# Kernel tuning notes

Hardware: AMD Instinct MI355X
Metric: run time of the kernel (lower is better)

## Reference

```python
import jax, jax.numpy as jnp
import numpy as np

NF = 64   # num_feat
DG = 8    # deformable_groups (also conv groups)
B, H, W = 4, 96, 96
K = 9     # 3x3 kernel positions


def _conv(x, w, b, padding=1, dilation=1, groups=1):
    out = jax.lax.conv_general_dilated(
        x, w, (1, 1), [(padding, padding), (padding, padding)],
        rhs_dilation=(dilation, dilation),
        dimension_numbers=('NCHW', 'OIHW', 'NCHW'),
        feature_group_count=groups)
    return out + b[None, :, None, None]


def _lrelu(t):
    return jnp.where(t >= 0, t, 0.1 * t)


def _cat_align(a, b):
    # channel-interleaved concat: [a0,b0,a1,b1,...]
    Bn, k, h, w = a.shape
    return jnp.stack([a, b], axis=2).reshape(Bn, 2 * k, h, w)


def _deform_conv(x, offset, mask, weight, bias, dilation, padding):
    # DCNv2 modulated deformable conv, stride 1.
    Bn, C, h, w = x.shape
    Cpg = C // DG
    off = offset.reshape(Bn, DG, K, 2, h, w)          # (dy, dx) per group/kernel pos
    m = mask.reshape(Bn, DG, K, h, w)
    ky = (jnp.repeat(jnp.arange(3), 3) * dilation - padding).astype(x.dtype)  # (K,)
    kx = (jnp.tile(jnp.arange(3), 3) * dilation - padding).astype(x.dtype)
    hs = jnp.arange(h, dtype=x.dtype)
    ws = jnp.arange(w, dtype=x.dtype)
    py = off[:, :, :, 0] + ky[None, None, :, None, None] + hs[None, None, None, :, None]
    px = off[:, :, :, 1] + kx[None, None, :, None, None] + ws[None, None, None, None, :]
    y0f = jnp.floor(py); x0f = jnp.floor(px)
    ly = (py - y0f)[:, :, None]  # broadcast over Cpg
    lx = (px - x0f)[:, :, None]
    y0 = y0f.astype(jnp.int32); x0 = x0f.astype(jnp.int32)
    xg = x.reshape(Bn, DG, Cpg, h * w)

    def gather(yi, xi):
        inb = ((yi >= 0) & (yi < h) & (xi >= 0) & (xi < w))
        idx = (jnp.clip(yi, 0, h - 1) * w + jnp.clip(xi, 0, w - 1)).reshape(Bn, DG, 1, K * h * w)
        v = jnp.take_along_axis(xg, jnp.broadcast_to(idx, (Bn, DG, Cpg, K * h * w)), axis=3)
        return v.reshape(Bn, DG, Cpg, K, h, w) * inb[:, :, None].astype(x.dtype)

    v00 = gather(y0, x0); v01 = gather(y0, x0 + 1)
    v10 = gather(y0 + 1, x0); v11 = gather(y0 + 1, x0 + 1)
    val = (v00 * (1 - ly) * (1 - lx) + v01 * (1 - ly) * lx
           + v10 * ly * (1 - lx) + v11 * ly * lx) * m[:, :, None]
    sampled = val.reshape(Bn, C, K, h, w)
    out = jnp.einsum('bckhw,ock->bohw', sampled, weight.reshape(weight.shape[0], C, K))
    return out + bias[None, :, None, None]


def _dcn(x, off_feat, om_w, om_b, w, b, dilation):
    pad = dilation  # int(3/2)*dilation
    out = _conv(off_feat, om_w, om_b, padding=pad, dilation=dilation)
    o1, o2, msk = jnp.split(out, 3, axis=1)
    offset = jnp.concatenate([o1, o2], axis=1)
    mask = jax.nn.sigmoid(msk)
    return _deform_conv(x, offset, mask, w, b, dilation, pad)


def setup_inputs() -> dict:
    key = jax.random.key(0)
    ks = iter(jax.random.split(key, 64))
    def rn(shape, s=0.05):
        return jax.random.normal(next(ks), shape, jnp.float32) * s
    d = {}
    d['nbr_feat'] = jax.random.normal(next(ks), (B, NF, H, W), jnp.float32)
    d['ref_feat'] = jax.random.normal(next(ks), (B, NF, H, W), jnp.float32)
    for lv, has3 in [('l3', False), ('l2', True), ('l1', True)]:
        d[f'oc1_w_{lv}'] = rn((NF, 2 * NF // DG, 3, 3)); d[f'oc1_b_{lv}'] = rn((NF,))
        oc2_in = 2 * NF if has3 else NF
        d[f'oc2_w_{lv}'] = rn((NF, oc2_in // DG, 3, 3)); d[f'oc2_b_{lv}'] = rn((NF,))
        if has3:
            d[f'oc3_w_{lv}'] = rn((NF, NF // DG, 3, 3)); d[f'oc3_b_{lv}'] = rn((NF,))
            d[f'fc_w_{lv}'] = rn((NF, 2 * NF // DG, 3, 3)); d[f'fc_b_{lv}'] = rn((NF,))
        d[f'om_w_{lv}'] = rn((DG * 3 * K, NF, 3, 3), 0.01); d[f'om_b_{lv}'] = rn((DG * 3 * K,), 0.01)
        d[f'dcn_w_{lv}'] = rn((NF, NF, 3, 3)); d[f'dcn_b_{lv}'] = rn((NF,))
    d['cas_oc1_w'] = rn((NF, 2 * NF // DG, 3, 3)); d['cas_oc1_b'] = rn((NF,))
    d['cas_oc2_w'] = rn((NF, NF // DG, 3, 3)); d['cas_oc2_b'] = rn((NF,))
    d['cas_om_w'] = rn((DG * 3 * K, NF, 3, 3), 0.01); d['cas_om_b'] = rn((DG * 3 * K,), 0.01)
    d['cas_w'] = rn((NF, NF, 3, 3)); d['cas_b'] = rn((NF,))
    return d


def reference(nbr_feat, ref_feat,
              oc1_w_l3, oc1_b_l3, oc2_w_l3, oc2_b_l3, om_w_l3, om_b_l3, dcn_w_l3, dcn_b_l3,
              oc1_w_l2, oc1_b_l2, oc2_w_l2, oc2_b_l2, oc3_w_l2, oc3_b_l2, fc_w_l2, fc_b_l2,
              om_w_l2, om_b_l2, dcn_w_l2, dcn_b_l2,
              oc1_w_l1, oc1_b_l1, oc2_w_l1, oc2_b_l1, oc3_w_l1, oc3_b_l1, fc_w_l1, fc_b_l1,
              om_w_l1, om_b_l1, dcn_w_l1, dcn_b_l1,
              cas_oc1_w, cas_oc1_b, cas_oc2_w, cas_oc2_b, cas_om_w, cas_om_b, cas_w, cas_b):
    # level 3 (dilation 5)
    off = _lrelu(_conv(_cat_align(nbr_feat, ref_feat), oc1_w_l3, oc1_b_l3, groups=DG))
    off = _lrelu(_conv(off, oc2_w_l3, oc2_b_l3, groups=DG))
    feat = _lrelu(_dcn(nbr_feat, off, om_w_l3, om_b_l3, dcn_w_l3, dcn_b_l3, 5))
    to, tf = off, feat
    # level 2 (dilation 3)
    off = _lrelu(_conv(_cat_align(nbr_feat, ref_feat), oc1_w_l2, oc1_b_l2, groups=DG))
    off = _lrelu(_conv(_cat_align(off, to), oc2_w_l2, oc2_b_l2, groups=DG))
    off = _lrelu(_conv(off, oc3_w_l2, oc3_b_l2, groups=DG))
    feat = _dcn(nbr_feat, off, om_w_l2, om_b_l2, dcn_w_l2, dcn_b_l2, 3)
    feat = _lrelu(_conv(_cat_align(feat, tf), fc_w_l2, fc_b_l2, groups=DG))
    to, tf = off, feat
    # level 1 (dilation 1), no lrelu on feat
    off = _lrelu(_conv(_cat_align(nbr_feat, ref_feat), oc1_w_l1, oc1_b_l1, groups=DG))
    off = _lrelu(_conv(_cat_align(off, to), oc2_w_l1, oc2_b_l1, groups=DG))
    off = _lrelu(_conv(off, oc3_w_l1, oc3_b_l1, groups=DG))
    feat = _dcn(nbr_feat, off, om_w_l1, om_b_l1, dcn_w_l1, dcn_b_l1, 1)
    feat = _conv(_cat_align(feat, tf), fc_w_l1, fc_b_l1, groups=DG)
    # cascade
    off = _cat_align(feat, ref_feat)
    off = _lrelu(_conv(_lrelu(_conv(off, cas_oc1_w, cas_oc1_b, groups=DG)), cas_oc2_w, cas_oc2_b, groups=DG))
    feat = _lrelu(_dcn(feat, off, cas_om_w, cas_om_b, cas_w, cas_b, 1))
    return feat
```

## Files before the change

kernel.cpp:

```cpp
#include <hip/hip_runtime.h>

#define BATCH 4
#define NFEAT 64
#define DGRP 8
#define HH 96
#define WW 96
#define HWP (HH*WW)

typedef short short4a __attribute__((ext_vector_type(4)));
typedef short short8 __attribute__((ext_vector_type(8)));
typedef float f32x4 __attribute__((ext_vector_type(4)));
typedef float f32x16 __attribute__((ext_vector_type(16)));

__device__ inline short f2bf(float f) {
  union { float f; unsigned u; } v; v.f = f;
  unsigned r = v.u + 0x7fff + ((v.u >> 16) & 1);
  return (short)(r >> 16);
}
__device__ inline float bf2f(short s) {
  return __uint_as_float(((unsigned)(unsigned short)s) << 16);
}

__global__ __launch_bounds__(256) void prep_om(
    const float* __restrict__ s0, const float* __restrict__ s1,
    const float* __restrict__ s2, const float* __restrict__ s3,
    short* __restrict__ dst) {
  int gid = blockIdx.x * 256 + threadIdx.x;
  if (gid >= 4 * 147456) return;
  int t = gid / 147456, r = gid % 147456;
  int tile = r / 18432, r2 = r % 18432;
  int kk = r2 / 512, r3 = r2 % 512;
  int lane = r3 / 8, j = r3 % 8;
  int col = lane & 31, half = lane >> 5;
  int oc = tile * 32 + col;
  int k = kk * 16 + half * 8 + j;
  int p = k >> 6, c = k & 63;
  const float* s = (t == 0) ? s0 : (t == 1) ? s1 : (t == 2) ? s2 : s3;
  float v = (oc < 216) ? s[(size_t)oc * 576 + c * 9 + p] : 0.f;
  dst[gid] = f2bf(v);
}

__global__ __launch_bounds__(256) void prep_dcnw(
    const float* __restrict__ s0, const float* __restrict__ s1,
    const float* __restrict__ s2, const float* __restrict__ s3,
    short* __restrict__ dst) {
  int gid = blockIdx.x * 256 + threadIdx.x;
  if (gid >= 4 * 36864) return;
  int t = gid / 36864, r = gid % 36864;
  int tile = r / 18432, r2 = r % 18432;
  int kk = r2 / 512, r3 = r2 % 512;
  int lane = r3 / 8, j = r3 % 8;
  int col = lane & 31, half = lane >> 5;
  int oc = tile * 32 + col;
  int k = kk * 16 + half * 8 + j;
  int p = k >> 6, c = k & 63;
  const float* s = (t == 0) ? s0 : (t == 1) ? s1 : (t == 2) ? s2 : s3;
  dst[gid] = f2bf(s[(size_t)oc * 576 + c * 9 + p]);
}

struct GwArgs {
  const float* src[12];
  int cat[12];
  int base[13];
};

__global__ __launch_bounds__(256) void prep_gw(GwArgs a, short* __restrict__ dst) {
  int gid = blockIdx.x * 256 + threadIdx.x;
  if (gid >= a.base[12]) return;
  int t = 0;
  while (gid >= a.base[t + 1]) ++t;
  int r = gid - a.base[t];
  const float* s = a.src[t];
  const int tsz = a.cat[t] ? 4608 : 2560;
  int tile = r / tsz, r2 = r % tsz;
  int kk = r2 / 512, r3 = r2 % 512;
  int lane = r3 >> 3, j = r3 & 7;
  int m = lane & 15, quad = lane >> 4;
  int oc = tile * 16 + m;
  int j32 = quad * 8 + j;
  float val = 0.f;
  if (a.cat[t]) {
    int gsel = j32 >> 4, ssel = (j32 >> 3) & 1, ch8 = j32 & 7;
    if (gsel == (m >> 3)) val = s[oc * 144 + (2 * ch8 + ssel) * 9 + kk];
  } else {
    int tapsel = j32 >> 4, gsel = (j32 >> 3) & 1, ch8 = j32 & 7;
    int p = 2 * kk + tapsel;
    if (p < 9 && gsel == (m >> 3)) val = s[oc * 72 + ch8 * 9 + p];
  }
  dst[gid] = f2bf(val);
}

__global__ __launch_bounds__(256) void transpose_bf16(
    const float* __restrict__ in0, short* __restrict__ out0,
    const float* __restrict__ in1, short* __restrict__ out1) {
  const float* in = blockIdx.z ? in1 : in0;
  short* out = blockIdx.z ? out1 : out0;
  __shared__ float s[64][65];
  const int p0 = blockIdx.x * 64;
  const int b = blockIdx.y;
  const int tx = threadIdx.x, ty = threadIdx.y;
  for (int c = ty; c < 64; c += 4)
    s[c][tx] = in[((size_t)b * NFEAT + c) * HWP + p0 + tx];
  __syncthreads();
  for (int p = ty; p < 64; p += 4)
    out[((size_t)b * HWP + p0 + p) * NFEAT + tx] = f2bf(s[tx][p]);
}

template <bool CAT, bool LRELU>
__device__ __forceinline__ void gconv_body(
    const short* __restrict__ in0, const short* __restrict__ in1,
    const short* __restrict__ Wsh, const float* __restrict__ bias,
    short* __restrict__ out, int pixbase, int b) {
  const int lane = threadIdx.x, t = threadIdx.y;
  const int n = lane & 15, quad = lane >> 4;
  constexpr int NKK = CAT ? 9 : 5;

  short8 A[NKK];
#pragma unroll
  for (int kk = 0; kk < NKK; ++kk)
    A[kk] = *(const short8*)(Wsh + ((size_t)(t * NKK + kk) * 64 + lane) * 8);

  const short* sb;
  if (CAT) {
    sb = ((quad & 1) ? in1 : in0) + (size_t)b * HWP * 64 + (2 * t + (quad >> 1)) * 8;
  } else {
    sb = in0 + (size_t)b * HWP * 64 + (2 * t + (quad & 1)) * 8;
  }

  f32x4 acc[2] = {};
#pragma unroll
  for (int nt = 0; nt < 2; ++nt) {
    const int pix = pixbase + nt * 16 + n;
    const int yp = pix / WW, xp = pix % WW;
#pragma unroll
    for (int kk = 0; kk < NKK; ++kk) {
      const int p = CAT ? kk : (2 * kk + (quad >> 1));
      short8 B = {0, 0, 0, 0, 0, 0, 0, 0};
      if (p < 9) {
        const int sy = yp + p / 3 - 1, sx = xp + p % 3 - 1;
        if (((unsigned)sy < (unsigned)HH) && ((unsigned)sx < (unsigned)WW))
          B = *(const short8*)(sb + (size_t)(sy * WW + sx) * 64);
      }
      acc[nt] = __builtin_amdgcn_mfma_f32_16x16x32_bf16(A[kk], B, acc[nt], 0, 0, 0);
    }
  }

  const int ocb = t * 16 + quad * 4;
  const float b0 = bias[ocb], b1 = bias[ocb + 1], b2 = bias[ocb + 2], b3 = bias[ocb + 3];
#pragma unroll
  for (int nt = 0; nt < 2; ++nt) {
    float v0 = acc[nt][0] + b0, v1 = acc[nt][1] + b1;
    float v2 = acc[nt][2] + b2, v3 = acc[nt][3] + b3;
    if (LRELU) {
      v0 = (v0 >= 0.f) ? v0 : 0.1f * v0;
      v1 = (v1 >= 0.f) ? v1 : 0.1f * v1;
      v2 = (v2 >= 0.f) ? v2 : 0.1f * v2;
      v3 = (v3 >= 0.f) ? v3 : 0.1f * v3;
    }
    short4a pk = {f2bf(v0), f2bf(v1), f2bf(v2), f2bf(v3)};
    *(short4a*)(out + ((size_t)b * HWP + pixbase + nt * 16 + n) * 64 + ocb) = pk;
  }
}

template <bool CAT, bool LRELU>
__global__ __launch_bounds__(256) void gconv_mfma(
    const short* __restrict__ in0, const short* __restrict__ in1,
    const short* __restrict__ Wsh, const float* __restrict__ bias,
    short* __restrict__ out) {
  gconv_body<CAT, LRELU>(in0, in1, Wsh, bias, out, blockIdx.x * 32, blockIdx.y);
}

struct Oc1Args {
  const short* W[3];
  const float* bias[3];
  short* out[3];
};

__global__ __launch_bounds__(256) void gconv_oc1x3(
    const short* __restrict__ in0, const short* __restrict__ in1, Oc1Args a) {
  const int job = blockIdx.z;
  gconv_body<true, true>(in0, in1, a.W[job], a.bias[job], a.out[job],
                         blockIdx.x * 32, blockIdx.y);
}

#define BPITCH 324
template <int D>
__global__ __launch_bounds__(256) void omconv_mfma(
    const short* __restrict__ pixT,
    const short* __restrict__ Wsh,
    const float* __restrict__ bias,
    short* __restrict__ out) {
  const int lane = threadIdx.x;
  const int w = threadIdx.y;
  const int lid = w * 64 + lane;
  const int col = lane & 31, half = lane >> 5;
  const int pixbase = blockIdx.x * 64;
  const int b = blockIdx.y;

  __shared__ short Bs[64 * BPITCH];

  const short* aP0 = Wsh + ((size_t)(w * 36) * 64) * 8 + (size_t)lane * 8;
  const short* aP1 = Wsh + ((size_t)((w + 4) * 36) * 64) * 8 + (size_t)lane * 8;
  const short* pixb = pixT + (size_t)b * HWP * 64;

  f32x16 acc00 = {}, acc01 = {}, acc10 = {}, acc11 = {};

  for (int ph = 0; ph < 2; ++ph) {
    const int ntap = ph ? 4 : 5, pbase = ph ? 5 : 0, kbase = ph ? 20 : 0;
    if (ph) __syncthreads();
    const int nchunk = 64 * ntap * 8;
    for (int i = lid; i < nchunk; i += 256) {
      int row = i / (ntap * 8), q = i % (ntap * 8);
      int p = pbase + (q >> 3), c8 = q & 7;
      int pix = pixbase + row;
      int yp = pix / WW, xp = pix % WW;
      int sy = yp + (p / 3 - 1) * D, sx = xp + (p % 3 - 1) * D;
      short4a lo = {0, 0, 0, 0}, hi = {0, 0, 0, 0};
      if (((unsigned)sy < (unsigned)HH) && ((unsigned)sx < (unsigned)WW)) {
        const short* src = pixb + (size_t)(sy * WW + sx) * 64 + c8 * 8;
        lo = *(const short4a*)src;
        hi = *(const short4a*)(src + 4);
      }
      short* dst = Bs + row * BPITCH + q * 8;
      *(short4a*)dst = lo;
      *(short4a*)(dst + 4) = hi;
    }
    __syncthreads();

    const int nkk = ntap * 4;
#pragma unroll 4
    for (int kk = 0; kk < nkk; ++kk) {
      const int kkg = kbase + kk;
      short8 A0 = *(const short8*)(aP0 + (size_t)kkg * 512);
      short8 A1 = *(const short8*)(aP1 + (size_t)kkg * 512);
      const short* b0 = Bs + col * BPITCH + kk * 16 + half * 8;
      const short* b1 = Bs + (32 + col) * BPITCH + kk * 16 + half * 8;
      short4a l0 = *(const short4a*)b0, h0 = *(const short4a*)(b0 + 4);
      short4a l1 = *(const short4a*)b1, h1 = *(const short4a*)(b1 + 4);
      short8 B0 = {l0[0], l0[1], l0[2], l0[3], h0[0], h0[1], h0[2], h0[3]};
      short8 B1 = {l1[0], l1[1], l1[2], l1[3], h1[0], h1[1], h1[2], h1[3]};
      acc00 = __builtin_amdgcn_mfma_f32_32x32x16_bf16(A0, B0, acc00, 0, 0, 0);
      acc01 = __builtin_amdgcn_mfma_f32_32x32x16_bf16(A0, B1, acc01, 0, 0, 0);
      acc10 = __builtin_amdgcn_mfma_f32_32x32x16_bf16(A1, B0, acc10, 0, 0, 0);
      acc11 = __builtin_amdgcn_mfma_f32_32x32x16_bf16(A1, B1, acc11, 0, 0, 0);
    }
  }

  const int pix0 = pixbase + col, pix1 = pixbase + 32 + col;
#pragma unroll
  for (int r = 0; r < 16; ++r) {
    const int rrow = (r & 3) + 8 * (r >> 2) + 4 * half;
    const int oc0 = w * 32 + rrow;
    const int oc1 = (w + 4) * 32 + rrow;
    const float bs0 = bias[oc0];
    out[((size_t)b * 216 + oc0) * HWP + pix0] = f2bf(acc00[r] + bs0);
    out[((size_t)b * 216 + oc0) * HWP + pix1] = f2bf(acc01[r] + bs0);
    if (oc1 < 216) {
      const float bs1 = bias[oc1];
      out[((size_t)b * 216 + oc1) * HWP + pix0] = f2bf(acc10[r] + bs1);
      out[((size_t)b * 216 + oc1) * HWP + pix1] = f2bf(acc11[r] + bs1);
    }
  }
}

template <int D, bool LRELU, bool PMOUT>
__global__ __launch_bounds__(256) void dcn_fused(
    const short* __restrict__ xT,
    const short* __restrict__ om,
    const short* __restrict__ Wd,
    const float* __restrict__ bias,
    void* __restrict__ outv) {
  __shared__ short Ls[36 * 512];
  __shared__ float red[2][64][17];
  const int tx = threadIdx.x, ty = threadIdx.y;
  const int pb = blockIdx.x, b = blockIdx.y;

  {
    const int px = tx, dg = ty;
    const int pix = pb * 32 + px;
    const int yp = pix / WW, xp = pix % WW;
    const size_t bOM = (size_t)b * 216 * HWP;
    const short* xb = xT + (size_t)b * HWP * 64 + dg * 8;
    short* Sp = Ls + (size_t)((dg & 1) * 32 + px) * 8;

#pragma unroll
    for (int k = 0; k < 9; ++k) {
      float dy = bf2f(om[bOM + (size_t)(dg * 18 + 2 * k) * HWP + pix]);
      float dxv = bf2f(om[bOM + (size_t)(dg * 18 + 2 * k + 1) * HWP + pix]);
      float mr = bf2f(om[bOM + (size_t)(144 + dg * 9 + k) * HWP + pix]);
      float m = 1.f / (1.f + __expf(-mr));
      float py = (float)(yp + (k / 3 - 1) * D) + dy;
      float px_ = (float)(xp + (k % 3 - 1) * D) + dxv;
      float y0f = floorf(py), x0f = floorf(px_);
      float ly = py - y0f, lx = px_ - x0f;
      int y0 = (int)y0f, x0 = (int)x0f;
      int y1 = y0 + 1, x1 = x0 + 1;
      bool vy0 = (unsigned)y0 < (unsigned)HH, vy1 = (unsigned)y1 < (unsigned)HH;
      bool vx0 = (unsigned)x0 < (unsigned)WW, vx1 = (unsigned)x1 < (unsigned)WW;
      int cy0 = min(max(y0, 0), HH - 1), cy1 = min(max(y1, 0), HH - 1);
      int cx0 = min(max(x0, 0), WW - 1), cx1 = min(max(x1, 0), WW - 1);
      float w00 = (vy0 && vx0) ? (1.f - ly) * (1.f - lx) * m : 0.f;
      float w01 = (vy0 && vx1) ? (1.f - ly) * lx * m : 0.f;
      float w10 = (vy1 && vx0) ? ly * (1.f - lx) * m : 0.f;
      float w11 = (vy1 && vx1) ? ly * lx * m : 0.f;
      short8 s00 = *(const short8*)(xb + (size_t)(cy0 * WW + cx0) * 64);
      short8 s01 = *(const short8*)(xb + (size_t)(cy0 * WW + cx1) * 64);
      short8 s10 = *(const short8*)(xb + (size_t)(cy1 * WW + cx0) * 64);
      short8 s11 = *(const short8*)(xb + (size_t)(cy1 * WW + cx1) * 64);
      short8 pk;
#pragma unroll
      for (int cl = 0; cl < 8; ++cl) {
        float v = w00 * bf2f(s00[cl]) + w01 * bf2f(s01[cl]) +
                  w10 * bf2f(s10[cl]) + w11 * bf2f(s11[cl]);
        pk[cl] = f2bf(v);
      }
      const int kk = k * 4 + (dg >> 1);
      *(short8*)(Sp + (size_t)kk * 512) = pk;
    }
  }
  __syncthreads();

  const int lid = ty * 32 + tx;
  const int lane = lid & 63, w = lid >> 6;
  const int col = lane & 31, half = lane >> 5;
  const int octile = w & 1, kh = w >> 1;
  const int pix = pb * 32 + col;

  const short* aP = Wd + ((size_t)(octile * 36) * 64 + lane) * 8;
  const short* bP = Ls + (size_t)lane * 8;

  f32x16 acc = {};
#pragma unroll 6
  for (int kk = 0; kk < 18; ++kk) {
    const int kkg = kh * 18 + kk;
    short8 A = *(const short8*)(aP + (size_t)kkg * 512);
    short8 B = *(const short8*)(bP + (size_t)kkg * 512);
    acc = __builtin_amdgcn_mfma_f32_32x32x16_bf16(A, B, acc, 0, 0, 0);
  }

  if (kh == 1) {
#pragma unroll
    for (int r = 0; r < 16; ++r) red[octile][lane][r] = acc[r];
  }
  __syncthreads();
  if (kh == 0) {
    if (PMOUT) {
      short* out = (short*)outv;
#pragma unroll
      for (int rg = 0; rg < 4; ++rg) {
        short4a pk;
#pragma unroll
        for (int i = 0; i < 4; ++i) {
          const int r = rg * 4 + i;
          const int oc = octile * 32 + i + 8 * rg + 4 * half;
          float v = acc[r] + red[octile][lane][r] + bias[oc];
          if (LRELU) v = (v >= 0.f) ? v : 0.1f * v;
          pk[i] = f2bf(v);
        }
        *(short4a*)(out + ((size_t)b * HWP + pix) * 64 + octile * 32 + 8 * rg + 4 * half) = pk;
      }
    } else {
      float* out = (float*)outv;
#pragma unroll
      for (int r = 0; r < 16; ++r) {
        const int oc = octile * 32 + (r & 3) + 8 * (r >> 2) + 4 * half;
        float v = acc[r] + red[octile][lane][r] + bias[oc];
        if (LRELU) v = (v >= 0.f) ? v : 0.1f * v;
        out[((size_t)b * NFEAT + oc) * HWP + pix] = v;
      }
    }
  }
}

extern "C" void kernel_launch(void* const* d_in, const int* in_sizes, int n_in,
                              void* d_out, int out_size, void* d_ws, size_t ws_size,
                              hipStream_t stream) {
  const float* nbr = (const float*)d_in[0];
  const float* ref = (const float*)d_in[1];
  auto f = [&](int i) { return (const float*)d_in[i]; };

  short* s0 = (short*)d_ws;
  const size_t PM = (size_t)BATCH * HWP * 64;
  short* omB = s0;
  short* refT = omB + 7962624;
  short* pmA = refT + PM;
  short* pmB = pmA + PM;
  short* pmC = pmB + PM;
  short* pmD = pmC + PM;
  short* pmE = pmD + PM;
  short* pmF = pmE + PM;
  short* pmG = pmF + PM;
  short* wbf = pmG + PM;
  short* wdcn = wbf + 589824;
  short* wgc = wdcn + 147456;
  short* nbrT = (short*)d_out;

  prep_om<<<(4 * 147456 + 255) / 256, 256, 0, stream>>>(f(6), f(18), f(30), f(38), wbf);
  prep_dcnw<<<(4 * 36864 + 255) / 256, 256, 0, stream>>>(f(8), f(20), f(32), f(40), wdcn);

  static const int gSrc[12] = {2, 4, 10, 12, 14, 16, 22, 24, 26, 28, 34, 36};
  static const int gCat[12] = {1, 0, 1, 1, 0, 1, 1, 1, 0, 1, 1, 0};
  GwArgs ga;
  int gb = 0;
  const short* wg[12];
  for (int t = 0; t < 12; ++t) {
    ga.src[t] = f(gSrc[t]);
    ga.cat[t] = gCat[t];
    ga.base[t] = gb;
    wg[t] = wgc + gb;
    gb += gCat[t] ? 18432 : 10240;
  }
  ga.base[12] = gb;
  prep_gw<<<(gb + 255) / 256, 256, 0, stream>>>(ga, wgc);

  short* wbf_l3 = wbf;
  short* wbf_l2 = wbf + 147456;
  short* wbf_l1 = wbf + 2 * 147456;
  short* wbf_cas = wbf + 3 * 147456;
  short* wd_l3 = wdcn;
  short* wd_l2 = wdcn + 36864;
  short* wd_l1 = wdcn + 2 * 36864;
  short* wd_cas = wdcn + 3 * 36864;

  dim3 gcGrid(288, BATCH), gcBlk(64, 4);
  dim3 oc1Grid(288, BATCH, 3);
  dim3 omGrid(144, BATCH), omBlk(64, 4);
  dim3 dfGrid(288, BATCH), dfBlk(32, 8);
  dim3 trGrid(HWP / 64, BATCH, 2), trBlk(64, 4);

  transpose_bf16<<<trGrid, trBlk, 0, stream>>>(nbr, nbrT, ref, refT);

  Oc1Args oa;
  oa.W[0] = wg[0]; oa.bias[0] = f(3);  oa.out[0] = pmA;
  oa.W[1] = wg[2]; oa.bias[1] = f(11); oa.out[1] = pmF;
  oa.W[2] = wg[6]; oa.bias[2] = f(23); oa.out[2] = pmG;
  gconv_oc1x3<<<oc1Grid, gcBlk, 0, stream>>>(nbrT, refT, oa);

  gconv_mfma<false, true><<<gcGrid, gcBlk, 0, stream>>>(pmA, nullptr, wg[1], f(5), pmB);
  omconv_mfma<5><<<omGrid, omBlk, 0, stream>>>(pmB, wbf_l3, f(7), omB);
  dcn_fused<5, true, true><<<dfGrid, dfBlk, 0, stream>>>(nbrT, omB, wd_l3, f(9), pmC);

  gconv_mfma<true, true><<<gcGrid, gcBlk, 0, stream>>>(pmF, pmB, wg[3], f(13), pmD);
  gconv_mfma<false, true><<<gcGrid, gcBlk, 0, stream>>>(pmD, nullptr, wg[4], f(15), pmE);
  omconv_mfma<3><<<omGrid, omBlk, 0, stream>>>(pmE, wbf_l2, f(19), omB);
  dcn_fused<3, false, true><<<dfGrid, dfBlk, 0, stream>>>(nbrT, omB, wd_l2, f(21), pmD);
  gconv_mfma<true, true><<<gcGrid, gcBlk, 0, stream>>>(pmD, pmC, wg[5], f(17), pmA);

  gconv_mfma<true, true><<<gcGrid, gcBlk, 0, stream>>>(pmG, pmE, wg[7], f(25), pmB);
  gconv_mfma<false, true><<<gcGrid, gcBlk, 0, stream>>>(pmB, nullptr, wg[8], f(27), pmC);
  omconv_mfma<1><<<omGrid, omBlk, 0, stream>>>(pmC, wbf_l1, f(31), omB);
  dcn_fused<1, false, true><<<dfGrid, dfBlk, 0, stream>>>(nbrT, omB, wd_l1, f(33), pmD);
  gconv_mfma<true, false><<<gcGrid, gcBlk, 0, stream>>>(pmD, pmA, wg[9], f(29), pmB);

  gconv_mfma<true, true><<<gcGrid, gcBlk, 0, stream>>>(pmB, refT, wg[10], f(35), pmC);
  gconv_mfma<false, true><<<gcGrid, gcBlk, 0, stream>>>(pmC, nullptr, wg[11], f(37), pmD);
  omconv_mfma<1><<<omGrid, omBlk, 0, stream>>>(pmD, wbf_cas, f(39), omB);
  dcn_fused<1, true, false><<<dfGrid, dfBlk, 0, stream>>>(pmB, omB, wd_cas, f(41), (float*)d_out);
}
```

Before: 526.7 us.

## Fuse offset/mask conv into deformable conv kernel via LDS handoff

Merges the separate offset/mask MFMA convolution kernel into the deformable conv kernel. Each 32-pixel block now computes its 216 offset/mask channels into shared memory and consumes them directly, instead of writing them to a global buffer and reading them back. This removes the global round trip of the 216-channel om tensor and one launch per level. In exchange, pixel tiles shrink from 64 to 32 per block for the om conv, so weight loads are reused less, and the larger shared footprint (about 51KB) may lower occupancy.

```diff
diff --git a/kernel.cpp b/kernel.cpp
--- a/kernel.cpp
+++ b/kernel.cpp
@@ -183,111 +183,93 @@
                          blockIdx.x * 32, blockIdx.y);
 }
 
-#define BPITCH 324
-template <int D>
-__global__ __launch_bounds__(256) void omconv_mfma(
-    const short* __restrict__ pixT,
-    const short* __restrict__ Wsh,
+#define OMPITCH 580
+#define OMLP 33
+
+template <int D, bool LRELU, bool PMOUT>
+__global__ __launch_bounds__(256) void omdcn_fused(
+    const short* __restrict__ omIn,
+    const short* __restrict__ xT,
+    const short* __restrict__ Wom,
+    const float* __restrict__ obias,
+    const short* __restrict__ Wd,
     const float* __restrict__ bias,
-    short* __restrict__ out) {
-  const int lane = threadIdx.x;
-  const int w = threadIdx.y;
-  const int lid = w * 64 + lane;
+    void* __restrict__ outv) {
+  __shared__ __align__(16) char smem[37120 + 14256];
+  short* Bs = (short*)smem;
+  short* Ls = (short*)smem;
+  short* om_lds = (short*)(smem + 37120);
+  float* red = (float*)(smem + 37120);
+
+  const int tx = threadIdx.x, ty = threadIdx.y;
+  const int lid = ty * 32 + tx;
+  const int lane = lid & 63, w = lid >> 6;
   const int col = lane & 31, half = lane >> 5;
-  const int pixbase = blockIdx.x * 64;
-  const int b = blockIdx.y;
-
-  __shared__ short Bs[64 * BPITCH];
-
-  const short* aP0 = Wsh + ((size_t)(w * 36) * 64) * 8 + (size_t)lane * 8;
-  const short* aP1 = Wsh + ((size_t)((w + 4) * 36) * 64) * 8 + (size_t)lane * 8;
-  const short* pixb = pixT + (size_t)b * HWP * 64;
-
-  f32x16 acc00 = {}, acc01 = {}, acc10 = {}, acc11 = {};
-
-  for (int ph = 0; ph < 2; ++ph) {
-    const int ntap = ph ? 4 : 5, pbase = ph ? 5 : 0, kbase = ph ? 20 : 0;
-    if (ph) __syncthreads();
-    const int nchunk = 64 * ntap * 8;
-    for (int i = lid; i < nchunk; i += 256) {
-      int row = i / (ntap * 8), q = i % (ntap * 8);
-      int p = pbase + (q >> 3), c8 = q & 7;
-      int pix = pixbase + row;
-      int yp = pix / WW, xp = pix % WW;
-      int sy = yp + (p / 3 - 1) * D, sx = xp + (p % 3 - 1) * D;
+  const int pb = blockIdx.x, b = blockIdx.y;
+  const int pixbase = pb * 32;
+
+  {
+    const short* pixb = omIn + (size_t)b * HWP * 64;
+#pragma unroll
+    for (int t = 0; t < 9; ++t) {
+      const int i = lid + t * 256;
+      const int row = i / 72, q = i % 72;
+      const int p = q >> 3, c8 = q & 7;
+      const int pix = pixbase + row;
+      const int yp = pix / WW, xp = pix % WW;
+      const int sy = yp + (p / 3 - 1) * D, sx = xp + (p % 3 - 1) * D;
       short4a lo = {0, 0, 0, 0}, hi = {0, 0, 0, 0};
       if (((unsigned)sy < (unsigned)HH) && ((unsigned)sx < (unsigned)WW)) {
         const short* src = pixb + (size_t)(sy * WW + sx) * 64 + c8 * 8;
         lo = *(const short4a*)src;
         hi = *(const short4a*)(src + 4);
       }
-      short* dst = Bs + row * BPITCH + q * 8;
+      short* dst = Bs + row * OMPITCH + q * 8;
       *(short4a*)dst = lo;
       *(short4a*)(dst + 4) = hi;
     }
-    __syncthreads();
-
-    const int nkk = ntap * 4;
+  }
+  __syncthreads();
+
+  {
+    const short* aP0 = Wom + ((size_t)(w * 36) * 64 + lane) * 8;
+    const short* aP1 = Wom + ((size_t)((w + 4) * 36) * 64 + lane) * 8;
+    const short* bbase = Bs + col * OMPITCH + half * 8;
+    f32x16 acc0 = {}, acc1 = {};
 #pragma unroll 4
-    for (int kk = 0; kk < nkk; ++kk) {
-      const int kkg = kbase + kk;
-      short8 A0 = *(const short8*)(aP0 + (size_t)kkg * 512);
-      short8 A1 = *(const short8*)(aP1 + (size_t)kkg * 512);
-      const short* b0 = Bs + col * BPITCH + kk * 16 + half * 8;
-      const short* b1 = Bs + (32 + col) * BPITCH + kk * 16 + half * 8;
-      short4a l0 = *(const short4a*)b0, h0 = *(const short4a*)(b0 + 4);
-      short4a l1 = *(const short4a*)b1, h1 = *(const short4a*)(b1 + 4);
-      short8 B0 = {l0[0], l0[1], l0[2], l0[3], h0[0], h0[1], h0[2], h0[3]};
-      short8 B1 = {l1[0], l1[1], l1[2], l1[3], h1[0], h1[1], h1[2], h1[3]};
-      acc00 = __builtin_amdgcn_mfma_f32_32x32x16_bf16(A0, B0, acc00, 0, 0, 0);
-      acc01 = __builtin_amdgcn_mfma_f32_32x32x16_bf16(A0, B1, acc01, 0, 0, 0);
-      acc10 = __builtin_amdgcn_mfma_f32_32x32x16_bf16(A1, B0, acc10, 0, 0, 0);
-      acc11 = __builtin_amdgcn_mfma_f32_32x32x16_bf16(A1, B1, acc11, 0, 0, 0);
-    }
-  }
-
-  const int pix0 = pixbase + col, pix1 = pixbase + 32 + col;
-#pragma unroll
-  for (int r = 0; r < 16; ++r) {
-    const int rrow = (r & 3) + 8 * (r >> 2) + 4 * half;
-    const int oc0 = w * 32 + rrow;
-    const int oc1 = (w + 4) * 32 + rrow;
-    const float bs0 = bias[oc0];
-    out[((size_t)b * 216 + oc0) * HWP + pix0] = f2bf(acc00[r] + bs0);
-    out[((size_t)b * 216 + oc0) * HWP + pix1] = f2bf(acc01[r] + bs0);
-    if (oc1 < 216) {
-      const float bs1 = bias[oc1];
-      out[((size_t)b * 216 + oc1) * HWP + pix0] = f2bf(acc10[r] + bs1);
-      out[((size_t)b * 216 + oc1) * HWP + pix1] = f2bf(acc11[r] + bs1);
-    }
-  }
-}
-
-template <int D, bool LRELU, bool PMOUT>
-__global__ __launch_bounds__(256) void dcn_fused(
-    const short* __restrict__ xT,
-    const short* __restrict__ om,
-    const short* __restrict__ Wd,
-    const float* __restrict__ bias,
-    void* __restrict__ outv) {
-  __shared__ short Ls[36 * 512];
-  __shared__ float red[2][64][17];
-  const int tx = threadIdx.x, ty = threadIdx.y;
-  const int pb = blockIdx.x, b = blockIdx.y;
+    for (int kk = 0; kk < 36; ++kk) {
+      const short* bp = bbase + kk * 16;
+      short4a l = *(const short4a*)bp, h = *(const short4a*)(bp + 4);
+      short8 B = {l[0], l[1], l[2], l[3], h[0], h[1], h[2], h[3]};
+      short8 A0 = *(const short8*)(aP0 + (size_t)kk * 512);
+      short8 A1 = *(const short8*)(aP1 + (size_t)kk * 512);
+      acc0 = __builtin_amdgcn_mfma_f32_32x32x16_bf16(A0, B, acc0, 0, 0, 0);
+      acc1 = __builtin_amdgcn_mfma_f32_32x32x16_bf16(A1, B, acc1, 0, 0, 0);
+    }
+#pragma unroll
+    for (int r = 0; r < 16; ++r) {
+      const int rrow = (r & 3) + 8 * (r >> 2) + 4 * half;
+      const int oc0 = w * 32 + rrow;
+      om_lds[oc0 * OMLP + col] = f2bf(acc0[r] + obias[oc0]);
+      const int oc1 = (w + 4) * 32 + rrow;
+      if (oc1 < 216)
+        om_lds[oc1 * OMLP + col] = f2bf(acc1[r] + obias[oc1]);
+    }
+  }
+  __syncthreads();
 
   {
     const int px = tx, dg = ty;
-    const int pix = pb * 32 + px;
+    const int pix = pixbase + px;
     const int yp = pix / WW, xp = pix % WW;
-    const size_t bOM = (size_t)b * 216 * HWP;
     const short* xb = xT + (size_t)b * HWP * 64 + dg * 8;
     short* Sp = Ls + (size_t)((dg & 1) * 32 + px) * 8;
 
 #pragma unroll
     for (int k = 0; k < 9; ++k) {
-      float dy = bf2f(om[bOM + (size_t)(dg * 18 + 2 * k) * HWP + pix]);
-      float dxv = bf2f(om[bOM + (size_t)(dg * 18 + 2 * k + 1) * HWP + pix]);
-      float mr = bf2f(om[bOM + (size_t)(144 + dg * 9 + k) * HWP + pix]);
+      float dy = bf2f(om_lds[(dg * 18 + 2 * k) * OMLP + px]);
+      float dxv = bf2f(om_lds[(dg * 18 + 2 * k + 1) * OMLP + px]);
+      float mr = bf2f(om_lds[(144 + dg * 9 + k) * OMLP + px]);
       float m = 1.f / (1.f + __expf(-mr));
       float py = (float)(yp + (k / 3 - 1) * D) + dy;
       float px_ = (float)(xp + (k % 3 - 1) * D) + dxv;
@@ -320,11 +302,8 @@
   }
   __syncthreads();
 
-  const int lid = ty * 32 + tx;
-  const int lane = lid & 63, w = lid >> 6;
-  const int col = lane & 31, half = lane >> 5;
   const int octile = w & 1, kh = w >> 1;
-  const int pix = pb * 32 + col;
+  const int pix = pixbase + col;
 
   const short* aP = Wd + ((size_t)(octile * 36) * 64 + lane) * 8;
   const short* bP = Ls + (size_t)lane * 8;
@@ -340,7 +319,7 @@
 
   if (kh == 1) {
 #pragma unroll
-    for (int r = 0; r < 16; ++r) red[octile][lane][r] = acc[r];
+    for (int r = 0; r < 16; ++r) red[(octile * 64 + lane) * 17 + r] = acc[r];
   }
   __syncthreads();
   if (kh == 0) {
@@ -353,7 +332,7 @@
         for (int i = 0; i < 4; ++i) {
           const int r = rg * 4 + i;
           const int oc = octile * 32 + i + 8 * rg + 4 * half;
-          float v = acc[r] + red[octile][lane][r] + bias[oc];
+          float v = acc[r] + red[(octile * 64 + lane) * 17 + r] + bias[oc];
           if (LRELU) v = (v >= 0.f) ? v : 0.1f * v;
           pk[i] = f2bf(v);
         }
@@ -364,7 +343,7 @@
 #pragma unroll
       for (int r = 0; r < 16; ++r) {
         const int oc = octile * 32 + (r & 3) + 8 * (r >> 2) + 4 * half;
-        float v = acc[r] + red[octile][lane][r] + bias[oc];
+        float v = acc[r] + red[(octile * 64 + lane) * 17 + r] + bias[oc];
         if (LRELU) v = (v >= 0.f) ? v : 0.1f * v;
         out[((size_t)b * NFEAT + oc) * HWP + pix] = v;
       }
@@ -424,8 +403,7 @@
 
   dim3 gcGrid(288, BATCH), gcBlk(64, 4);
   dim3 oc1Grid(288, BATCH, 3);
-  dim3 omGrid(144, BATCH), omBlk(64, 4);
-  dim3 dfGrid(288, BATCH), dfBlk(32, 8);
+  dim3 fGrid(288, BATCH), fBlk(32, 8);
   dim3 trGrid(HWP / 64, BATCH, 2), trBlk(64, 4);
 
   transpose_bf16<<<trGrid, trBlk, 0, stream>>>(nbr, nbrT, ref, refT);
@@ -437,23 +415,23 @@
   gconv_oc1x3<<<oc1Grid, gcBlk, 0, stream>>>(nbrT, refT, oa);
 
   gconv_mfma<false, true><<<gcGrid, gcBlk, 0, stream>>>(pmA, nullptr, wg[1], f(5), pmB);
-  omconv_mfma<5><<<omGrid, omBlk, 0, stream>>>(pmB, wbf_l3, f(7), omB);
-  dcn_fused<5, true, true><<<dfGrid, dfBlk, 0, stream>>>(nbrT, omB, wd_l3, f(9), pmC);
+  omdcn_fused<5, true, true><<<fGrid, fBlk, 0, stream>>>(
+      pmB, nbrT, wbf_l3, f(7), wd_l3, f(9), pmC);
 
   gconv_mfma<true, true><<<gcGrid, gcBlk, 0, stream>>>(pmF, pmB, wg[3], f(13), pmD);
   gconv_mfma<false, true><<<gcGrid, gcBlk, 0, stream>>>(pmD, nullptr, wg[4], f(15), pmE);
-  omconv_mfma<3><<<omGrid, omBlk, 0, stream>>>(pmE, wbf_l2, f(19), omB);
-  dcn_fused<3, false, true><<<dfGrid, dfBlk, 0, stream>>>(nbrT, omB, wd_l2, f(21), pmD);
+  omdcn_fused<3, false, true><<<fGrid, fBlk, 0, stream>>>(
+      pmE, nbrT, wbf_l2, f(19), wd_l2, f(21), pmD);
   gconv_mfma<true, true><<<gcGrid, gcBlk, 0, stream>>>(pmD, pmC, wg[5], f(17), pmA);
 
   gconv_mfma<true, true><<<gcGrid, gcBlk, 0, stream>>>(pmG, pmE, wg[7], f(25), pmB);
   gconv_mfma<false, true><<<gcGrid, gcBlk, 0, stream>>>(pmB, nullptr, wg[8], f(27), pmC);
-  omconv_mfma<1><<<omGrid, omBlk, 0, stream>>>(pmC, wbf_l1, f(31), omB);
-  dcn_fused<1, false, true><<<dfGrid, dfBlk, 0, stream>>>(nbrT, omB, wd_l1, f(33), pmD);
+  omdcn_fused<1, false, true><<<fGrid, fBlk, 0, stream>>>(
+      pmC, nbrT, wbf_l1, f(31), wd_l1, f(33), pmD);
   gconv_mfma<true, false><<<gcGrid, gcBlk, 0, stream>>>(pmD, pmA, wg[9], f(29), pmB);
 
   gconv_mfma<true, true><<<gcGrid, gcBlk, 0, stream>>>(pmB, refT, wg[10], f(35), pmC);
   gconv_mfma<false, true><<<gcGrid, gcBlk, 0, stream>>>(pmC, nullptr, wg[11], f(37), pmD);
-  omconv_mfma<1><<<omGrid, omBlk, 0, stream>>>(pmD, wbf_cas, f(39), omB);
-  dcn_fused<1, true, false><<<dfGrid, dfBlk, 0, stream>>>(pmB, omB, wd_cas, f(41), (float*)d_out);
-}
+  omdcn_fused<1, true, false><<<fGrid, fBlk, 0, stream>>>(
+      pmD, pmB, wbf_cas, f(39), wd_cas, f(41), (float*)d_out);
+}
```

New measurement: 546.1 us. 3.7% more time.

## Prefetch second omconv tap phase into registers; merge two independent gconvs into one launch

Applied to the files above, without the earlier changes.

The offset/mask conv kernel now issues the global loads for the second group of taps into registers before computing on the first group. Those values are written to shared memory only after the first MFMA phase, so load latency overlaps with compute. A custom barrier waits only on LDS counters and leaves global loads in flight. Separately, the level-2 feature conv and the level-1 offset conv are independent, so they now run as one launch split by blockIdx.z, removing a launch and letting their blocks share the GPU. The register prefetch adds VGPR pressure that could lower occupancy.

```diff
diff --git a/kernel.cpp b/kernel.cpp
--- a/kernel.cpp
+++ b/kernel.cpp
@@ -19,6 +19,12 @@
 }
 __device__ inline float bf2f(short s) {
   return __uint_as_float(((unsigned)(unsigned short)s) << 16);
+}
+
+__device__ __forceinline__ void barrier_keep_vmcnt() {
+  asm volatile("s_waitcnt lgkmcnt(0)" ::: "memory");
+  __builtin_amdgcn_s_barrier();
+  asm volatile("" ::: "memory");
 }
 
 __global__ __launch_bounds__(256) void prep_om(
@@ -183,6 +189,20 @@
                          blockIdx.x * 32, blockIdx.y);
 }
 
+struct Pair2Args {
+  const short* in0[2];
+  const short* in1[2];
+  const short* W[2];
+  const float* bias[2];
+  short* out[2];
+};
+
+__global__ __launch_bounds__(256) void gconv_pair(Pair2Args a) {
+  const int j = blockIdx.z;
+  gconv_body<true, true>(a.in0[j], a.in1[j], a.W[j], a.bias[j], a.out[j],
+                         blockIdx.x * 32, blockIdx.y);
+}
+
 #define BPITCH 324
 template <int D>
 __global__ __launch_bounds__(256) void omconv_mfma(
@@ -205,45 +225,85 @@
 
   f32x16 acc00 = {}, acc01 = {}, acc10 = {}, acc11 = {};
 
-  for (int ph = 0; ph < 2; ++ph) {
-    const int ntap = ph ? 4 : 5, pbase = ph ? 5 : 0, kbase = ph ? 20 : 0;
-    if (ph) __syncthreads();
-    const int nchunk = 64 * ntap * 8;
-    for (int i = lid; i < nchunk; i += 256) {
-      int row = i / (ntap * 8), q = i % (ntap * 8);
-      int p = pbase + (q >> 3), c8 = q & 7;
-      int pix = pixbase + row;
-      int yp = pix / WW, xp = pix % WW;
-      int sy = yp + (p / 3 - 1) * D, sx = xp + (p % 3 - 1) * D;
-      short4a lo = {0, 0, 0, 0}, hi = {0, 0, 0, 0};
-      if (((unsigned)sy < (unsigned)HH) && ((unsigned)sx < (unsigned)WW)) {
-        const short* src = pixb + (size_t)(sy * WW + sx) * 64 + c8 * 8;
-        lo = *(const short4a*)src;
-        hi = *(const short4a*)(src + 4);
-      }
-      short* dst = Bs + row * BPITCH + q * 8;
-      *(short4a*)dst = lo;
-      *(short4a*)(dst + 4) = hi;
-    }
-    __syncthreads();
-
-    const int nkk = ntap * 4;
+  for (int i = lid; i < 64 * 5 * 8; i += 256) {
+    int row = i / 40, q = i % 40;
+    int p = q >> 3, c8 = q & 7;
+    int pix = pixbase + row;
+    int yp = pix / WW, xp = pix % WW;
+    int sy = yp + (p / 3 - 1) * D, sx = xp + (p % 3 - 1) * D;
+    short4a lo = {0, 0, 0, 0}, hi = {0, 0, 0, 0};
+    if (((unsigned)sy < (unsigned)HH) && ((unsigned)sx < (unsigned)WW)) {
+      const short* src = pixb + (size_t)(sy * WW + sx) * 64 + c8 * 8;
+      lo = *(const short4a*)src;
+      hi = *(const short4a*)(src + 4);
+    }
+    short* dst = Bs + row * BPITCH + q * 8;
+    *(short4a*)dst = lo;
+    *(short4a*)(dst + 4) = hi;
+  }
+
+  short4a p1lo[8], p1hi[8];
+  int p1dst[8];
+#pragma unroll
+  for (int idx = 0; idx < 8; ++idx) {
+    int i = lid + idx * 256;
+    int row = i / 32, q = i % 32;
+    int p = 5 + (q >> 3), c8 = q & 7;
+    int pix = pixbase + row;
+    int yp = pix / WW, xp = pix % WW;
+    int sy = yp + (p / 3 - 1) * D, sx = xp + (p % 3 - 1) * D;
+    short4a lo = {0, 0, 0, 0}, hi = {0, 0, 0, 0};
+    if (((unsigned)sy < (unsigned)HH) && ((unsigned)sx < (unsigned)WW)) {
+      const short* src = pixb + (size_t)(sy * WW + sx) * 64 + c8 * 8;
+      lo = *(const short4a*)src;
+      hi = *(const short4a*)(src + 4);
+    }
+    p1lo[idx] = lo;
+    p1hi[idx] = hi;
+    p1dst[idx] = row * BPITCH + q * 8;
+  }
+  barrier_keep_vmcnt();
+
 #pragma unroll 4
-    for (int kk = 0; kk < nkk; ++kk) {
-      const int kkg = kbase + kk;
-      short8 A0 = *(const short8*)(aP0 + (size_t)kkg * 512);
-      short8 A1 = *(const short8*)(aP1 + (size_t)kkg * 512);
-      const short* b0 = Bs + col * BPITCH + kk * 16 + half * 8;
-      const short* b1 = Bs + (32 + col) * BPITCH + kk * 16 + half * 8;
-      short4a l0 = *(const short4a*)b0, h0 = *(const short4a*)(b0 + 4);
-      short4a l1 = *(const short4a*)b1, h1 = *(const short4a*)(b1 + 4);
-      short8 B0 = {l0[0], l0[1], l0[2], l0[3], h0[0], h0[1], h0[2], h0[3]};
-      short8 B1 = {l1[0], l1[1], l1[2], l1[3], h1[0], h1[1], h1[2], h1[3]};
-      acc00 = __builtin_amdgcn_mfma_f32_32x32x16_bf16(A0, B0, acc00, 0, 0, 0);
-      acc01 = __builtin_amdgcn_mfma_f32_32x32x16_bf16(A0, B1, acc01, 0, 0, 0);
-      acc10 = __builtin_amdgcn_mfma_f32_32x32x16_bf16(A1, B0, acc10, 0, 0, 0);
-      acc11 = __builtin_amdgcn_mfma_f32_32x32x16_bf16(A1, B1, acc11, 0, 0, 0);
-    }
+  for (int kk = 0; kk < 20; ++kk) {
+    short8 A0 = *(const short8*)(aP0 + (size_t)kk * 512);
+    short8 A1 = *(const short8*)(aP1 + (size_t)kk * 512);
+    const short* b0 = Bs + col * BPITCH + kk * 16 + half * 8;
+    const short* b1 = Bs + (32 + col) * BPITCH + kk * 16 + half * 8;
+    short4a l0 = *(const short4a*)b0, h0 = *(const short4a*)(b0 + 4);
+    short4a l1 = *(const short4a*)b1, h1 = *(const short4a*)(b1 + 4);
+    short8 B0 = {l0[0], l0[1], l0[2], l0[3], h0[0], h0[1], h0[2], h0[3]};
+    short8 B1 = {l1[0], l1[1], l1[2], l1[3], h1[0], h1[1], h1[2], h1[3]};
+    acc00 = __builtin_amdgcn_mfma_f32_32x32x16_bf16(A0, B0, acc00, 0, 0, 0);
+    acc01 = __builtin_amdgcn_mfma_f32_32x32x16_bf16(A0, B1, acc01, 0, 0, 0);
+    acc10 = __builtin_amdgcn_mfma_f32_32x32x16_bf16(A1, B0, acc10, 0, 0, 0);
+    acc11 = __builtin_amdgcn_mfma_f32_32x32x16_bf16(A1, B1, acc11, 0, 0, 0);
+  }
+  barrier_keep_vmcnt();
+
+#pragma unroll
+  for (int idx = 0; idx < 8; ++idx) {
+    short* dst = Bs + p1dst[idx];
+    *(short4a*)dst = p1lo[idx];
+    *(short4a*)(dst + 4) = p1hi[idx];
+  }
+  barrier_keep_vmcnt();
+
+#pragma unroll 4
+  for (int kk = 0; kk < 16; ++kk) {
+    const int kkg = 20 + kk;
+    short8 A0 = *(const short8*)(aP0 + (size_t)kkg * 512);
+    short8 A1 = *(const short8*)(aP1 + (size_t)kkg * 512);
+    const short* b0 = Bs + col * BPITCH + kk * 16 + half * 8;
+    const short* b1 = Bs + (32 + col) * BPITCH + kk * 16 + half * 8;
+    short4a l0 = *(const short4a*)b0, h0 = *(const short4a*)(b0 + 4);
+    short4a l1 = *(const short4a*)b1, h1 = *(const short4a*)(b1 + 4);
+    short8 B0 = {l0[0], l0[1], l0[2], l0[3], h0[0], h0[1], h0[2], h0[3]};
+    short8 B1 = {l1[0], l1[1], l1[2], l1[3], h1[0], h1[1], h1[2], h1[3]};
+    acc00 = __builtin_amdgcn_mfma_f32_32x32x16_bf16(A0, B0, acc00, 0, 0, 0);
+    acc01 = __builtin_amdgcn_mfma_f32_32x32x16_bf16(A0, B1, acc01, 0, 0, 0);
+    acc10 = __builtin_amdgcn_mfma_f32_32x32x16_bf16(A1, B0, acc10, 0, 0, 0);
+    acc11 = __builtin_amdgcn_mfma_f32_32x32x16_bf16(A1, B1, acc11, 0, 0, 0);
   }
 
   const int pix0 = pixbase + col, pix1 = pixbase + 32 + col;
@@ -424,6 +484,7 @@
 
   dim3 gcGrid(288, BATCH), gcBlk(64, 4);
   dim3 oc1Grid(288, BATCH, 3);
+  dim3 pairGrid(288, BATCH, 2);
   dim3 omGrid(144, BATCH), omBlk(64, 4);
   dim3 dfGrid(288, BATCH), dfBlk(32, 8);
   dim3 trGrid(HWP / 64, BATCH, 2), trBlk(64, 4);
@@ -444,9 +505,12 @@
   gconv_mfma<false, true><<<gcGrid, gcBlk, 0, stream>>>(pmD, nullptr, wg[4], f(15), pmE);
   omconv_mfma<3><<<omGrid, omBlk, 0, stream>>>(pmE, wbf_l2, f(19), omB);
   dcn_fused<3, false, true><<<dfGrid, dfBlk, 0, stream>>>(nbrT, omB, wd_l2, f(21), pmD);
-  gconv_mfma<true, true><<<gcGrid, gcBlk, 0, stream>>>(pmD, pmC, wg[5], f(17), pmA);
-
-  gconv_mfma<true, true><<<gcGrid, gcBlk, 0, stream>>>(pmG, pmE, wg[7], f(25), pmB);
+
+  Pair2Args pa;
+  pa.in0[0] = pmD; pa.in1[0] = pmC; pa.W[0] = wg[5]; pa.bias[0] = f(17); pa.out[0] = pmA;
+  pa.in0[1] = pmG; pa.in1[1] = pmE; pa.W[1] = wg[7]; pa.bias[1] = f(25); pa.out[1] = pmB;
+  gconv_pair<<<pairGrid, gcBlk, 0, stream>>>(pa);
+
   gconv_mfma<false, true><<<gcGrid, gcBlk, 0, stream>>>(pmB, nullptr, wg[8], f(27), pmC);
   omconv_mfma<1><<<omGrid, omBlk, 0, stream>>>(pmC, wbf_l1, f(31), omB);
   dcn_fused<1, false, true><<<dfGrid, dfBlk, 0, stream>>>(nbrT, omB, wd_l1, f(33), pmD);
```

Result: no change. 517.1 us (-1.8%).
